# Kernel tuning notes

Measured on AMD Instinct MI355X. Metric: run time of the kernel, lower is better.

## Reference

```python
import jax, jax.numpy as jnp
import numpy as np

DIM = 768
HEADS = 12
HEAD_DIM = DIM // HEADS
EPS_ATTN = 1e-6
LN_EPS = 1e-5


def _piece_weight():
    # BlockDistanceConv with num_patches_per_side=16, patch_group_size=16 -> 4x4 blocks
    bps = 4
    centers = np.array([[i + 0.5, j + 0.5] for i in range(bps) for j in range(bps)], dtype=np.float32)
    d = np.linalg.norm(centers[:, None, :] - centers[None, :, :], axis=-1)
    mat = np.cos(d / d.max() * np.pi / 4.0)  # 'cos' transform
    mat = mat / mat.sum(axis=0, keepdims=True)
    return jnp.asarray(mat, dtype=jnp.float32)  # [16, 16], out = W @ x over piece channels


def setup_inputs() -> dict:
    key = jax.random.key(0)
    ks = jax.random.split(key, 4)
    B, N, W, C = 128, 16, 16, DIM
    x = jax.random.normal(ks[0], (B, N, W, C), dtype=jnp.float32)
    ln_gamma = jnp.ones((C,), dtype=jnp.float32)
    ln_beta = jnp.zeros((C,), dtype=jnp.float32)
    w_qkv = jax.random.normal(ks[1], (C, 3 * C), dtype=jnp.float32) * (C ** -0.5)
    w_out = jax.random.normal(ks[2], (C, C), dtype=jnp.float32) * (C ** -0.5)
    b_out = jnp.zeros((C,), dtype=jnp.float32)
    w_piece = _piece_weight()
    return {"x": x, "ln_gamma": ln_gamma, "ln_beta": ln_beta, "w_qkv": w_qkv,
            "w_out": w_out, "b_out": b_out, "w_piece": w_piece}


def reference(x, ln_gamma, ln_beta, w_qkv, w_out, b_out, w_piece):
    B, N, W, C = x.shape
    H, D = HEADS, HEAD_DIM
    # LayerNorm over channel dim
    mu = jnp.mean(x, axis=-1, keepdims=True)
    var = jnp.mean((x - mu) ** 2, axis=-1, keepdims=True)
    xn = (x - mu) * jax.lax.rsqrt(var + LN_EPS) * ln_gamma + ln_beta
    # qkv projection (no bias)
    qkv = xn @ w_qkv  # [B,N,W,3C]
    q, k, v = jnp.split(qkv, 3, axis=-1)
    # relu kernel feature map
    q = jax.nn.relu(q) + EPS_ATTN
    k = jax.nn.relu(k) + EPS_ATTN
    # split heads: 'b n w (h d) -> b h n w d'
    def heads(t):
        return t.reshape(B, N, W, H, D).transpose(0, 3, 1, 2, 4)
    q, k, v = heads(q), heads(k), heads(v)
    # per-window kv = k^T v  (sum over window positions w)  -> [B,H,N,D,D]
    kv = jnp.einsum('bhnwd,bhnwe->bhnde', k, v)
    # BlockDistanceConv: 1x1 conv mixing over piece dim N with fixed weights
    kv = jnp.einsum('ij,bhjde->bhide', w_piece, kv)
    # out = q @ kv  -> [B,H,N,W,D]
    out = jnp.einsum('bhnwd,bhnde->bhnwe', q, kv)
    # merge heads: 'b h n w d -> b n w (h d)'
    out = out.transpose(0, 2, 3, 1, 4).reshape(B, N, W, H * D)
    # output projection (dropout is identity in eval)
    return out @ w_out + b_out
```

## Files before the change

### kernel.cpp

```cpp
#include <hip/hip_runtime.h>

#define DIM 768
#define HEADS 12
#define TOK 32768

typedef unsigned short ushort_t;
typedef __attribute__((ext_vector_type(8))) short short8v;
typedef __attribute__((ext_vector_type(4))) float f32x4;
typedef __attribute__((ext_vector_type(4))) unsigned short us4;

__device__ __forceinline__ ushort_t f2bf(float x) {
  union { float f; unsigned u; } c; c.f = x;
  unsigned r = (c.u + 0x7FFFu + ((c.u >> 16) & 1u)) >> 16;
  return (ushort_t)r;
}

__device__ __forceinline__ void gload_lds16(const void* g, void* l) {
  __builtin_amdgcn_global_load_lds((const __attribute__((address_space(1))) void*)g,
                                   (__attribute__((address_space(3))) void*)l, 16, 0, 0);
}

#define FENCE asm volatile("" ::: "memory")
#define BARRIER do { FENCE; __builtin_amdgcn_s_barrier(); FENCE; } while (0)
#define LGK0 asm volatile("s_waitcnt lgkmcnt(0)" ::: "memory")

__global__ __launch_bounds__(256) void ln_kernel(const float* __restrict__ x,
                                                 const float* __restrict__ g,
                                                 const float* __restrict__ be,
                                                 ushort_t* __restrict__ xn) {
  int t = blockIdx.x;
  int tid = threadIdx.x;
  const float* row = x + (size_t)t * DIM;
  float v0 = row[tid], v1 = row[tid + 256], v2 = row[tid + 512];
  float s  = v0 + v1 + v2;
  float sq = v0 * v0 + v1 * v1 + v2 * v2;
  #pragma unroll
  for (int off = 32; off; off >>= 1) {
    s  += __shfl_down(s, off);
    sq += __shfl_down(sq, off);
  }
  __shared__ float ls[4], lq[4];
  int wid = tid >> 6, lane = tid & 63;
  if (lane == 0) { ls[wid] = s; lq[wid] = sq; }
  __syncthreads();
  s  = ls[0] + ls[1] + ls[2] + ls[3];
  sq = lq[0] + lq[1] + lq[2] + lq[3];
  float mu  = s * (1.0f / DIM);
  float var = sq * (1.0f / DIM) - mu * mu;
  float rs  = rsqrtf(var + 1e-5f);
  ushort_t* orow = xn + (size_t)t * DIM;
  orow[tid]       = f2bf((v0 - mu) * rs * g[tid]       + be[tid]);
  orow[tid + 256] = f2bf((v1 - mu) * rs * g[tid + 256] + be[tid + 256]);
  orow[tid + 512] = f2bf((v2 - mu) * rs * g[tid + 512] + be[tid + 512]);
}

__global__ __launch_bounds__(256) void convT(const float* __restrict__ src,
                                             ushort_t* __restrict__ dst, int R, int Ccol) {
  __shared__ float tile[32][33];
  int c0 = blockIdx.x * 32, r0 = blockIdx.y * 32;
  int tx = threadIdx.x & 31, ty = threadIdx.x >> 5;
  #pragma unroll
  for (int i = 0; i < 32; i += 8)
    tile[ty + i][tx] = src[(size_t)(r0 + ty + i) * Ccol + c0 + tx];
  __syncthreads();
  #pragma unroll
  for (int i = 0; i < 32; i += 8)
    dst[(size_t)(c0 + ty + i) * R + r0 + tx] = f2bf(tile[tx][ty + i]);
}

__global__ __launch_bounds__(512, 2) void gemm_8ph(const ushort_t* __restrict__ A,
                                                   const ushort_t* __restrict__ Bt,
                                                   ushort_t* __restrict__ qbf,
                                                   ushort_t* __restrict__ kbf,
                                                   ushort_t* __restrict__ vTbf) {
  extern __shared__ __align__(16) char lds[];
  const int Kb = DIM * 2;
  const int N = 3 * DIM;
  const int nbn = N / 256;
  const size_t GHalf = (size_t)64 * Kb;

  int bid = blockIdx.x;
  int qd = gridDim.x >> 3;
  int wid = (bid & 7) * qd + (bid >> 3);
  int bm = wid / nbn, bn = wid % nbn;
  int row0 = bm * 256, col0 = bn * 256;
  int t = threadIdx.x;
  int lane = t & 63, wave = t >> 6;
  int wr = wave >> 2, wc = wave & 3;

  const char* Ag = (const char*)A + (size_t)row0 * Kb;
  const char* Bg = (const char*)Bt + (size_t)col0 * Kb;

  int o0 = t * 16;
  int sr = o0 >> 7;
  int skb = (o0 & 127) ^ ((sr & 7) << 4);
  size_t goff = (size_t)sr * Kb + skb;

  #define STG(Gbase, Lbase, kt)                                               \
    do {                                                                      \
      gload_lds16((Gbase) + goff + (size_t)(kt) * 128, lds + (Lbase) + o0);   \
      gload_lds16((Gbase) + goff + GHalf + (size_t)(kt) * 128,                \
                  lds + (Lbase) + o0 + 8192);                                 \
    } while (0)

  int fr = lane & 15, fkb = (lane >> 4) << 4;
  int swz = (fr & 7) << 4;
  int kb0 = fkb ^ swz;
  int kb1 = (64 + fkb) ^ swz;
  int laA = (wr * 128 + fr) * 128;
  int laB = 32768 + (wc * 64 + fr) * 128;

  #define LOAD_A(dst, dbase, mq)                                              \
    _Pragma("unroll") for (int mi = 0; mi < 4; ++mi) {                        \
      dst[mi][0] = *(const short8v*)(lds + (dbase) + laA + (mq)*8192 + mi*2048 + kb0); \
      dst[mi][1] = *(const short8v*)(lds + (dbase) + laA + (mq)*8192 + mi*2048 + kb1); \
    }
  #define LOAD_B(dst, dbase, nq)                                              \
    _Pragma("unroll") for (int ni = 0; ni < 2; ++ni) {                        \
      dst[ni][0] = *(const short8v*)(lds + (dbase) + laB + (nq)*4096 + ni*2048 + kb0); \
      dst[ni][1] = *(const short8v*)(lds + (dbase) + laB + (nq)*4096 + ni*2048 + kb1); \
    }
  #define MFMA16(av, bv, mq, nq)                                              \
    do {                                                                      \
      __builtin_amdgcn_s_setprio(1);                                          \
      _Pragma("unroll") for (int mi = 0; mi < 4; ++mi)                        \
        _Pragma("unroll") for (int ni = 0; ni < 2; ++ni) {                    \
          acc[(mq)*4+mi][(nq)*2+ni] = __builtin_amdgcn_mfma_f32_16x16x32_bf16(\
              av[mi][0], bv[ni][0], acc[(mq)*4+mi][(nq)*2+ni], 0, 0, 0);      \
          acc[(mq)*4+mi][(nq)*2+ni] = __builtin_amdgcn_mfma_f32_16x16x32_bf16(\
              av[mi][1], bv[ni][1], acc[(mq)*4+mi][(nq)*2+ni], 0, 0, 0);      \
        }                                                                     \
      __builtin_amdgcn_s_setprio(0);                                          \
    } while (0)

  STG(Ag, 0, 0);  STG(Ag + 128 * Kb, 16384, 0);
  STG(Bg, 32768, 0);  STG(Bg + 128 * Kb, 49152, 0);
  STG(Ag, 65536, 1);  STG(Ag + 128 * Kb, 65536 + 16384, 1);
  STG(Bg, 65536 + 32768, 1);
  asm volatile("s_waitcnt vmcnt(6)" ::: "memory");
  __builtin_amdgcn_s_barrier();
  FENCE;

  short8v aR0[4][2], aR1[4][2], bR0[2][2], bR1[2][2];
  LOAD_A(aR0, 0, 0); LOAD_B(bR0, 0, 0);

  f32x4 acc[8][4] = {};
  for (int it = 0; it < 6; ++it) {
    const int d0 = 0, d1 = 65536;
    int t1k = 2 * it + 1, t2k = 2 * it + 2, t3k = 2 * it + 3;
    bool st = (it < 5);
    LOAD_A(aR1, d0, 1);
    STG(Bg + 128 * Kb, d1 + 49152, t1k);
    MFMA16(aR0, bR0, 0, 0);
    BARRIER;
    LOAD_B(bR1, d0, 1);
    MFMA16(aR1, bR0, 1, 0);
    BARRIER;
    if (st) { STG(Ag, d0, t2k); STG(Ag + 128 * Kb, d0 + 16384, t2k); }
    MFMA16(aR0, bR1, 0, 1);
    if (st) asm volatile("s_waitcnt vmcnt(4)" ::: "memory");
    else    asm volatile("s_waitcnt vmcnt(0)" ::: "memory");
    BARRIER;
    LOAD_A(aR0, d1, 0); LOAD_B(bR0, d1, 0);
    if (st) STG(Bg, d0 + 32768, t2k);
    MFMA16(aR1, bR1, 1, 1);
    BARRIER;
    LOAD_A(aR1, d1, 1);
    if (st) STG(Bg + 128 * Kb, d0 + 49152, t2k);
    MFMA16(aR0, bR0, 0, 0);
    BARRIER;
    LOAD_B(bR1, d1, 1);
    MFMA16(aR1, bR0, 1, 0);
    BARRIER;
    if (st) { STG(Ag, d1, t3k); STG(Ag + 128 * Kb, d1 + 16384, t3k); }
    MFMA16(aR0, bR1, 0, 1);
    if (st) asm volatile("s_waitcnt vmcnt(4)" ::: "memory");
    BARRIER;
    if (st) {
      LOAD_A(aR0, d0, 0); LOAD_B(bR0, d0, 0);
      STG(Bg, d1 + 32768, t3k);
    }
    MFMA16(aR1, bR1, 1, 1);
    BARRIER;
  }
  #undef STG
  #undef LOAD_A
  #undef LOAD_B
  #undef MFMA16

  int rbase = row0 + wr * 128 + ((lane >> 4) << 2);
  int cbase = col0 + wc * 64 + fr;
  #pragma unroll
  for (int m = 0; m < 8; ++m) {
    int r0r = rbase + m * 16;
    #pragma unroll
    for (int n = 0; n < 4; ++n) {
      int c = cbase + n * 16;
      if (c < DIM) {
        #pragma unroll
        for (int j = 0; j < 4; ++j)
          qbf[(size_t)(r0r + j) * DIM + c] = f2bf(fmaxf(acc[m][n][j], 0.0f) + 1e-6f);
      } else if (c < 2 * DIM) {
        #pragma unroll
        for (int j = 0; j < 4; ++j)
          kbf[(size_t)(r0r + j) * DIM + (c - DIM)] = f2bf(fmaxf(acc[m][n][j], 0.0f) + 1e-6f);
      } else {
        int ch = c - 2 * DIM;
        int hh = ch >> 6, e = ch & 63;
        int bb = r0r >> 8, rr = r0r & 255;
        us4 pk;
        #pragma unroll
        for (int j = 0; j < 4; ++j) pk[j] = f2bf(acc[m][n][j]);
        *(us4*)&vTbf[((((size_t)bb * HEADS + hh) * 64 + e) << 8) + rr] = pk;
      }
    }
  }
}

__global__ __launch_bounds__(512, 2) void gemm_out8(const ushort_t* __restrict__ A,
                                                    const ushort_t* __restrict__ Bt,
                                                    const float* __restrict__ bias,
                                                    float* __restrict__ C) {
  extern __shared__ __align__(16) char lds[];
  const int Kb = DIM * 2;
  const int N = DIM;
  const int nbn = N / 128;
  const size_t GHalf = (size_t)64 * Kb;

  int bid = blockIdx.x;
  int qd = gridDim.x >> 3;
  int wid = (bid & 7) * qd + (bid >> 3);
  int bm = wid / nbn, bn = wid % nbn;
  int row0 = bm * 256, col0 = bn * 128;
  int t = threadIdx.x;
  int lane = t & 63, wave = t >> 6;
  int wr = wave >> 2, wc = wave & 3;

  const char* Ag = (const char*)A + (size_t)row0 * Kb;
  const char* Bg = (const char*)Bt + (size_t)col0 * Kb;

  int o0 = t * 16;
  int sr = o0 >> 7;
  int skb = (o0 & 127) ^ ((sr & 7) << 4);
  size_t goff = (size_t)sr * Kb + skb;

  #define STGA(Gbase, Lbase, kt)                                              \
    do {                                                                      \
      gload_lds16((Gbase) + goff + (size_t)(kt) * 128, lds + (Lbase) + o0);   \
      gload_lds16((Gbase) + goff + GHalf + (size_t)(kt) * 128,                \
                  lds + (Lbase) + o0 + 8192);                                 \
    } while (0)
  #define STGB(Gbase, Lbase, kt)                                              \
    gload_lds16((Gbase) + goff + (size_t)(kt) * 128, lds + (Lbase) + o0)

  int fr = lane & 15, fkb = (lane >> 4) << 4;
  int swz = (fr & 7) << 4;
  int kb0 = fkb ^ swz;
  int kb1 = (64 + fkb) ^ swz;
  int laA = (wr * 128 + fr) * 128;
  int laB = 32768 + (wc * 32 + fr) * 128;

  #define LOAD_A(dst, dbase, mq)                                              \
    _Pragma("unroll") for (int mi = 0; mi < 4; ++mi) {                        \
      dst[mi][0] = *(const short8v*)(lds + (dbase) + laA + (mq)*8192 + mi*2048 + kb0); \
      dst[mi][1] = *(const short8v*)(lds + (dbase) + laA + (mq)*8192 + mi*2048 + kb1); \
    }
  #define LOAD_B(dst, dbase, nq)                                              \
    do {                                                                      \
      dst[0] = *(const short8v*)(lds + (dbase) + laB + (nq)*2048 + kb0);      \
      dst[1] = *(const short8v*)(lds + (dbase) + laB + (nq)*2048 + kb1);      \
    } while (0)
  #define MFMA8(av, bv, mq, nq)                                               \
    do {                                                                      \
      __builtin_amdgcn_s_setprio(1);                                          \
      _Pragma("unroll") for (int mi = 0; mi < 4; ++mi) {                      \
        acc[(mq)*4+mi][nq] = __builtin_amdgcn_mfma_f32_16x16x32_bf16(         \
            av[mi][0], bv[0], acc[(mq)*4+mi][nq], 0, 0, 0);                   \
        acc[(mq)*4+mi][nq] = __builtin_amdgcn_mfma_f32_16x16x32_bf16(         \
            av[mi][1], bv[1], acc[(mq)*4+mi][nq], 0, 0, 0);                   \
      }                                                                       \
      __builtin_amdgcn_s_setprio(0);                                          \
    } while (0)

  STGA(Ag, 0, 0);  STGA(Ag + 128 * Kb, 16384, 0);
  STGB(Bg, 32768, 0);  STGB(Bg + GHalf, 32768 + 8192, 0);
  STGA(Ag, 49152, 1);  STGA(Ag + 128 * Kb, 49152 + 16384, 1);
  STGB(Bg, 49152 + 32768, 1);
  asm volatile("s_waitcnt vmcnt(5)" ::: "memory");
  __builtin_amdgcn_s_barrier();
  FENCE;

  short8v aR0[4][2], aR1[4][2], bR0[2], bR1[2];
  LOAD_A(aR0, 0, 0); LOAD_B(bR0, 0, 0);

  f32x4 acc[8][2] = {};
  for (int it = 0; it < 6; ++it) {
    const int d0 = 0, d1 = 49152;
    int t1k = 2 * it + 1, t2k = 2 * it + 2, t3k = 2 * it + 3;
    bool st = (it < 5);
    LOAD_A(aR1, d0, 1);
    STGB(Bg + GHalf, d1 + 32768 + 8192, t1k);
    MFMA8(aR0, bR0, 0, 0);
    BARRIER;
    LOAD_B(bR1, d0, 1);
    MFMA8(aR1, bR0, 1, 0);
    BARRIER;
    if (st) { STGA(Ag, d0, t2k); STGA(Ag + 128 * Kb, d0 + 16384, t2k); }
    MFMA8(aR0, bR1, 0, 1);
    if (st) asm volatile("s_waitcnt vmcnt(4)" ::: "memory");
    else    asm volatile("s_waitcnt vmcnt(0)" ::: "memory");
    BARRIER;
    LOAD_A(aR0, d1, 0); LOAD_B(bR0, d1, 0);
    if (st) STGB(Bg, d0 + 32768, t2k);
    MFMA8(aR1, bR1, 1, 1);
    BARRIER;
    LOAD_A(aR1, d1, 1);
    if (st) STGB(Bg + GHalf, d0 + 32768 + 8192, t2k);
    MFMA8(aR0, bR0, 0, 0);
    BARRIER;
    LOAD_B(bR1, d1, 1);
    MFMA8(aR1, bR0, 1, 0);
    BARRIER;
    if (st) { STGA(Ag, d1, t3k); STGA(Ag + 128 * Kb, d1 + 16384, t3k); }
    MFMA8(aR0, bR1, 0, 1);
    if (st) asm volatile("s_waitcnt vmcnt(4)" ::: "memory");
    BARRIER;
    if (st) {
      LOAD_A(aR0, d0, 0); LOAD_B(bR0, d0, 0);
      STGB(Bg, d1 + 32768, t3k);
    }
    MFMA8(aR1, bR1, 1, 1);
    BARRIER;
  }
  #undef STGA
  #undef STGB
  #undef LOAD_A
  #undef LOAD_B
  #undef MFMA8

  int rbase = row0 + wr * 128 + ((lane >> 4) << 2);
  int cbase = col0 + wc * 32 + fr;
  #pragma unroll
  for (int m = 0; m < 8; ++m) {
    #pragma unroll
    for (int n = 0; n < 2; ++n) {
      int c = cbase + n * 16;
      float bz = bias[c];
      #pragma unroll
      for (int j = 0; j < 4; ++j)
        C[(size_t)(rbase + m * 16 + j) * N + c] = acc[m][n][j] + bz;
    }
  }
}

__global__ __launch_bounds__(512) void attn_fused(const ushort_t* __restrict__ qbf,
                                                  const ushort_t* __restrict__ kbf,
                                                  const ushort_t* __restrict__ vTbf,
                                                  const float* __restrict__ wp,
                                                  ushort_t* __restrict__ attnO) {
  extern __shared__ __align__(16) char lds[];
  const int QOFF = 65536, SOFF = 73728;
  int bh = blockIdx.x;
  int b = bh / HEADS, h = bh % HEADS;
  int t = threadIdx.x;
  int lane = t & 63, wave = t >> 6;
  int fr = lane & 15, fkb = (lane >> 4) << 4;
  int lg4 = (lane >> 4) << 2;

  const char* qg = (const char*)(qbf + ((size_t)b * 256) * DIM + h * 64);
  const char* kg = (const char*)(kbf + ((size_t)b * 256) * DIM + h * 64);
  const char* vg = (const char*)(vTbf + ((size_t)bh << 14));

  #pragma unroll
  for (int is = 0; is < 4; ++is) {
    int o = is * 8192 + t * 16;
    int r = o >> 7;
    int byt = (o & 127) ^ ((r & 7) << 4);
    gload_lds16(kg + (size_t)r * (DIM * 2) + byt, lds + o);
  }
  #pragma unroll
  for (int is = 0; is < 4; ++is) {
    int o = is * 8192 + t * 16;
    int e = o >> 9;
    int byt = (o & 511) ^ ((e & 7) << 4);
    gload_lds16(vg + e * 512 + byt, lds + 32768 + o);
  }
  {
    int o = t * 16;
    int r = o >> 7;
    int byt = (o & 127) ^ ((r & 7) << 4);
    gload_lds16(qg + (size_t)r * (DIM * 2) + byt, lds + QOFF + o);
  }
  asm volatile("s_waitcnt vmcnt(0)" ::: "memory");
  __builtin_amdgcn_s_barrier();

  int wrs = wave & 3, wcs = wave >> 2;
  int wrp = wave >> 2, wcp = wave & 3;

  for (int q4 = 0; q4 < 4; ++q4) {
    f32x4 accA[4][2] = {};
    {
      short8v kf[4][2], qf[2][2];
      #pragma unroll
      for (int mi = 0; mi < 4; ++mi)
        #pragma unroll
        for (int ks = 0; ks < 2; ++ks) {
          int r = wrs * 64 + mi * 16 + fr;
          kf[mi][ks] = *(const short8v*)(lds + r * 128 + ((ks * 64 + fkb) ^ ((r & 7) << 4)));
        }
      #pragma unroll
      for (int ni = 0; ni < 2; ++ni)
        #pragma unroll
        for (int ks = 0; ks < 2; ++ks) {
          int r = wcs * 32 + ni * 16 + fr;
          qf[ni][ks] = *(const short8v*)(lds + QOFF + r * 128 + ((ks * 64 + fkb) ^ ((r & 7) << 4)));
        }
      #pragma unroll
      for (int mi = 0; mi < 4; ++mi)
        #pragma unroll
        for (int ni = 0; ni < 2; ++ni)
          #pragma unroll
          for (int ks = 0; ks < 2; ++ks)
            accA[mi][ni] = __builtin_amdgcn_mfma_f32_16x16x32_bf16(kf[mi][ks], qf[ni][ks],
                                                                   accA[mi][ni], 0, 0, 0);
    }
    BARRIER;
    #pragma unroll
    for (int mi = 0; mi < 4; ++mi)
      #pragma unroll
      for (int ni = 0; ni < 2; ++ni) {
        float wpf = wp[(q4 * 4 + wcs * 2 + ni) * 16 + wrs * 4 + mi];
        us4 pk;
        #pragma unroll
        for (int j = 0; j < 4; ++j) pk[j] = f2bf(accA[mi][ni][j] * wpf);
        int qrow = wcs * 32 + ni * 16 + fr;
        int sbyte = (wrs * 64 + mi * 16 + lg4) * 2;
        *(us4*)(lds + SOFF + qrow * 512 + (sbyte ^ ((qrow & 7) << 4))) = pk;
      }
    if (q4 < 3) {
      int o = t * 16;
      int r = o >> 7;
      int byt = (o & 127) ^ ((r & 7) << 4);
      gload_lds16(qg + (size_t)((q4 + 1) * 64 + r) * (DIM * 2) + byt, lds + QOFF + o);
    }
    LGK0;
    BARRIER;
    f32x4 accB[2] = {{0.f,0.f,0.f,0.f},{0.f,0.f,0.f,0.f}};
    #pragma unroll
    for (int ks = 0; ks < 8; ++ks) {
      int kb = ks * 64 + fkb;
      int e = wcp * 16 + fr;
      short8v bv = *(const short8v*)(lds + 32768 + e * 512 + (kb ^ ((e & 7) << 4)));
      #pragma unroll
      for (int mt = 0; mt < 2; ++mt) {
        int r = wrp * 32 + mt * 16 + fr;
        short8v av = *(const short8v*)(lds + SOFF + r * 512 + (kb ^ ((r & 7) << 4)));
        accB[mt] = __builtin_amdgcn_mfma_f32_16x16x32_bf16(av, bv, accB[mt], 0, 0, 0);
      }
    }
    #pragma unroll
    for (int mt = 0; mt < 2; ++mt) {
      int row = b * 256 + q4 * 64 + wrp * 32 + mt * 16 + lg4;
      int col = h * 64 + wcp * 16 + fr;
      #pragma unroll
      for (int j = 0; j < 4; ++j)
        attnO[(size_t)(row + j) * DIM + col] = f2bf(accB[mt][j]);
    }
    if (q4 < 3) asm volatile("s_waitcnt vmcnt(8)" ::: "memory");
    BARRIER;
  }
}

extern "C" void kernel_launch(void* const* d_in, const int* in_sizes, int n_in,
                              void* d_out, int out_size, void* d_ws, size_t ws_size,
                              hipStream_t stream) {
  const float* x    = (const float*)d_in[0];
  const float* g    = (const float*)d_in[1];
  const float* be   = (const float*)d_in[2];
  const float* wqkv = (const float*)d_in[3];
  const float* wout = (const float*)d_in[4];
  const float* bout = (const float*)d_in[5];
  const float* wp   = (const float*)d_in[6];
  float* out = (float*)d_out;

  char* w = (char*)d_ws;
  const size_t SZ = (size_t)TOK * DIM * 2;
  ushort_t* qbf   = (ushort_t*)(w);
  ushort_t* kbf   = (ushort_t*)(w + SZ);
  ushort_t* vTbf  = (ushort_t*)(w + 2 * SZ);
  ushort_t* xn    = (ushort_t*)(w + 3 * SZ);
  ushort_t* wqkvT = (ushort_t*)(w + 4 * SZ);
  ushort_t* woutT = (ushort_t*)(w + 4 * SZ + 3538944);
  ushort_t* attnO = xn;

  (void)hipFuncSetAttribute(reinterpret_cast<const void*>(&gemm_8ph),
                            hipFuncAttributeMaxDynamicSharedMemorySize, 131072);
  (void)hipFuncSetAttribute(reinterpret_cast<const void*>(&gemm_out8),
                            hipFuncAttributeMaxDynamicSharedMemorySize, 98304);
  (void)hipFuncSetAttribute(reinterpret_cast<const void*>(&attn_fused),
                            hipFuncAttributeMaxDynamicSharedMemorySize, 106496);

  dim3 gt1(3 * DIM / 32, DIM / 32);
  convT<<<gt1, 256, 0, stream>>>(wqkv, wqkvT, DIM, 3 * DIM);
  dim3 gt2(DIM / 32, DIM / 32);
  convT<<<gt2, 256, 0, stream>>>(wout, woutT, DIM, DIM);

  ln_kernel<<<TOK, 256, 0, stream>>>(x, g, be, xn);

  gemm_8ph<<<(TOK / 256) * (3 * DIM / 256), 512, 131072, stream>>>(
      xn, wqkvT, qbf, kbf, vTbf);

  attn_fused<<<128 * HEADS, 512, 106496, stream>>>(qbf, kbf, vTbf, wp, attnO);

  gemm_out8<<<(TOK / 256) * (DIM / 128), 512, 98304, stream>>>(
      attnO, woutT, bout, out);
}
```

Before: 306.0 us.

## Vectorize LayerNorm per-wave, merge weight transposes, add sched barriers, overlap V load

The LayerNorm kernel now handles one row per wave with float4 loads and xor shuffles, so the shared-memory reduction and block sync go away. The two weight-transpose launches are merged into one kernel with a z-dimension. sched_barrier markers are added around barriers and MFMA groups in both GEMMs to stop the compiler reordering across them. In the attention kernel the Q load is issued before V and the first wait only covers K and Q, so the V load overlaps the first compute phase. The cost is more complex waitcnt bookkeeping and less freedom for the scheduler.

```diff
diff --git a/kernel.cpp b/kernel.cpp
--- a/kernel.cpp
+++ b/kernel.cpp
@@ -21,41 +21,59 @@
 }
 
 #define FENCE asm volatile("" ::: "memory")
-#define BARRIER do { FENCE; __builtin_amdgcn_s_barrier(); FENCE; } while (0)
+#define SCHED0 __builtin_amdgcn_sched_barrier(0)
+#define BARRIER do { FENCE; SCHED0; __builtin_amdgcn_s_barrier(); SCHED0; FENCE; } while (0)
 #define LGK0 asm volatile("s_waitcnt lgkmcnt(0)" ::: "memory")
 
 __global__ __launch_bounds__(256) void ln_kernel(const float* __restrict__ x,
                                                  const float* __restrict__ g,
                                                  const float* __restrict__ be,
                                                  ushort_t* __restrict__ xn) {
-  int t = blockIdx.x;
-  int tid = threadIdx.x;
-  const float* row = x + (size_t)t * DIM;
-  float v0 = row[tid], v1 = row[tid + 256], v2 = row[tid + 512];
-  float s  = v0 + v1 + v2;
-  float sq = v0 * v0 + v1 * v1 + v2 * v2;
+  int lane = threadIdx.x & 63;
+  int row = blockIdx.x * 4 + (threadIdx.x >> 6);
+  const float4* rx = (const float4*)(x + (size_t)row * DIM);
+  float4 v[3];
+  float s = 0.f, sq = 0.f;
+  #pragma unroll
+  for (int c = 0; c < 3; ++c) {
+    v[c] = rx[lane + 64 * c];
+    s  += v[c].x + v[c].y + v[c].z + v[c].w;
+    sq += v[c].x * v[c].x + v[c].y * v[c].y + v[c].z * v[c].z + v[c].w * v[c].w;
+  }
   #pragma unroll
   for (int off = 32; off; off >>= 1) {
-    s  += __shfl_down(s, off);
-    sq += __shfl_down(sq, off);
-  }
-  __shared__ float ls[4], lq[4];
-  int wid = tid >> 6, lane = tid & 63;
-  if (lane == 0) { ls[wid] = s; lq[wid] = sq; }
-  __syncthreads();
-  s  = ls[0] + ls[1] + ls[2] + ls[3];
-  sq = lq[0] + lq[1] + lq[2] + lq[3];
+    s  += __shfl_xor(s, off);
+    sq += __shfl_xor(sq, off);
+  }
   float mu  = s * (1.0f / DIM);
   float var = sq * (1.0f / DIM) - mu * mu;
   float rs  = rsqrtf(var + 1e-5f);
-  ushort_t* orow = xn + (size_t)t * DIM;
-  orow[tid]       = f2bf((v0 - mu) * rs * g[tid]       + be[tid]);
-  orow[tid + 256] = f2bf((v1 - mu) * rs * g[tid + 256] + be[tid + 256]);
-  orow[tid + 512] = f2bf((v2 - mu) * rs * g[tid + 512] + be[tid + 512]);
-}
-
-__global__ __launch_bounds__(256) void convT(const float* __restrict__ src,
-                                             ushort_t* __restrict__ dst, int R, int Ccol) {
+  us4* orow = (us4*)(xn + (size_t)row * DIM);
+  const float4* gv = (const float4*)g;
+  const float4* bv = (const float4*)be;
+  #pragma unroll
+  for (int c = 0; c < 3; ++c) {
+    float4 gg = gv[lane + 64 * c];
+    float4 bb = bv[lane + 64 * c];
+    us4 pk;
+    pk[0] = f2bf((v[c].x - mu) * rs * gg.x + bb.x);
+    pk[1] = f2bf((v[c].y - mu) * rs * gg.y + bb.y);
+    pk[2] = f2bf((v[c].z - mu) * rs * gg.z + bb.z);
+    pk[3] = f2bf((v[c].w - mu) * rs * gg.w + bb.w);
+    orow[lane + 64 * c] = pk;
+  }
+}
+
+__global__ __launch_bounds__(256) void convT2(const float* __restrict__ s0,
+                                              ushort_t* __restrict__ d0,
+                                              const float* __restrict__ s1,
+                                              ushort_t* __restrict__ d1) {
+  int z = blockIdx.z;
+  if (z && blockIdx.x >= DIM / 32) return;
+  const float* src = z ? s1 : s0;
+  ushort_t* dst = z ? d1 : d0;
+  int Ccol = z ? DIM : 3 * DIM;
+  const int R = DIM;
   __shared__ float tile[32][33];
   int c0 = blockIdx.x * 32, r0 = blockIdx.y * 32;
   int tx = threadIdx.x & 31, ty = threadIdx.x >> 5;
@@ -122,6 +140,7 @@
     }
   #define MFMA16(av, bv, mq, nq)                                              \
     do {                                                                      \
+      SCHED0;                                                                 \
       __builtin_amdgcn_s_setprio(1);                                          \
       _Pragma("unroll") for (int mi = 0; mi < 4; ++mi)                        \
         _Pragma("unroll") for (int ni = 0; ni < 2; ++ni) {                    \
@@ -138,8 +157,7 @@
   STG(Ag, 65536, 1);  STG(Ag + 128 * Kb, 65536 + 16384, 1);
   STG(Bg, 65536 + 32768, 1);
   asm volatile("s_waitcnt vmcnt(6)" ::: "memory");
-  __builtin_amdgcn_s_barrier();
-  FENCE;
+  BARRIER;
 
   short8v aR0[4][2], aR1[4][2], bR0[2][2], bR1[2][2];
   LOAD_A(aR0, 0, 0); LOAD_B(bR0, 0, 0);
@@ -272,6 +290,7 @@
     } while (0)
   #define MFMA8(av, bv, mq, nq)                                               \
     do {                                                                      \
+      SCHED0;                                                                 \
       __builtin_amdgcn_s_setprio(1);                                          \
       _Pragma("unroll") for (int mi = 0; mi < 4; ++mi) {                      \
         acc[(mq)*4+mi][nq] = __builtin_amdgcn_mfma_f32_16x16x32_bf16(         \
@@ -287,8 +306,7 @@
   STGA(Ag, 49152, 1);  STGA(Ag + 128 * Kb, 49152 + 16384, 1);
   STGB(Bg, 49152 + 32768, 1);
   asm volatile("s_waitcnt vmcnt(5)" ::: "memory");
-  __builtin_amdgcn_s_barrier();
-  FENCE;
+  BARRIER;
 
   short8v aR0[4][2], aR1[4][2], bR0[2], bR1[2];
   LOAD_A(aR0, 0, 0); LOAD_B(bR0, 0, 0);
@@ -378,6 +396,12 @@
     int byt = (o & 127) ^ ((r & 7) << 4);
     gload_lds16(kg + (size_t)r * (DIM * 2) + byt, lds + o);
   }
+  {
+    int o = t * 16;
+    int r = o >> 7;
+    int byt = (o & 127) ^ ((r & 7) << 4);
+    gload_lds16(qg + (size_t)r * (DIM * 2) + byt, lds + QOFF + o);
+  }
   #pragma unroll
   for (int is = 0; is < 4; ++is) {
     int o = is * 8192 + t * 16;
@@ -385,13 +409,7 @@
     int byt = (o & 511) ^ ((e & 7) << 4);
     gload_lds16(vg + e * 512 + byt, lds + 32768 + o);
   }
-  {
-    int o = t * 16;
-    int r = o >> 7;
-    int byt = (o & 127) ^ ((r & 7) << 4);
-    gload_lds16(qg + (size_t)r * (DIM * 2) + byt, lds + QOFF + o);
-  }
-  asm volatile("s_waitcnt vmcnt(0)" ::: "memory");
+  asm volatile("s_waitcnt vmcnt(4)" ::: "memory");
   __builtin_amdgcn_s_barrier();
 
   int wrs = wave & 3, wcs = wave >> 2;
@@ -445,6 +463,7 @@
     }
     LGK0;
     BARRIER;
+    if (q4 == 0) asm volatile("s_waitcnt vmcnt(1)" ::: "memory");
     f32x4 accB[2] = {{0.f,0.f,0.f,0.f},{0.f,0.f,0.f,0.f}};
     #pragma unroll
     for (int ks = 0; ks < 8; ++ks) {
@@ -500,12 +519,10 @@
   (void)hipFuncSetAttribute(reinterpret_cast<const void*>(&attn_fused),
                             hipFuncAttributeMaxDynamicSharedMemorySize, 106496);
 
-  dim3 gt1(3 * DIM / 32, DIM / 32);
-  convT<<<gt1, 256, 0, stream>>>(wqkv, wqkvT, DIM, 3 * DIM);
-  dim3 gt2(DIM / 32, DIM / 32);
-  convT<<<gt2, 256, 0, stream>>>(wout, woutT, DIM, DIM);
-
-  ln_kernel<<<TOK, 256, 0, stream>>>(x, g, be, xn);
+  dim3 gct(3 * DIM / 32, DIM / 32, 2);
+  convT2<<<gct, 256, 0, stream>>>(wqkv, wqkvT, wout, woutT);
+
+  ln_kernel<<<TOK / 4, 256, 0, stream>>>(x, g, be, xn);
 
   gemm_8ph<<<(TOK / 256) * (3 * DIM / 256), 512, 131072, stream>>>(
       xn, wqkvT, qbf, kbf, vTbf);
```

Measured after the change: 288.1 us. 5.9% less time.
